# Optimization experiments

Measured on AMD Instinct MI355X. Metric: run time of the kernel, lower is better.

Reference implementation:

```python
import jax, jax.numpy as jnp
import numpy as np

B, T, V, E, H, L = 32, 128, 32000, 256, 256, 2


def setup_inputs() -> dict:
    key = jax.random.key(0)
    ks = jax.random.split(key, 9)
    s = 0.05  # weight scale to keep gates out of deep saturation
    x = jax.random.randint(ks[0], (B, T), 0, V, dtype=jnp.int32)
    return {
        "x": x,
        "embed_table": jax.random.normal(ks[1], (V, E), jnp.float32) * 0.1,
        "fW": jax.random.normal(ks[2], (L, E, 4 * H), jnp.float32) * s,
        "fU": jax.random.normal(ks[3], (L, H, 4 * H), jnp.float32) * s,
        "fb": jnp.zeros((L, 4 * H), jnp.float32),
        "bW": jax.random.normal(ks[4], (L, E, 4 * H), jnp.float32) * s,
        "bU": jax.random.normal(ks[5], (L, H, 4 * H), jnp.float32) * s,
        "bb": jnp.zeros((L, 4 * H), jnp.float32),
        "Wp": jax.random.normal(ks[6], (2 * H, V), jnp.float32) * s,
        "bp": jnp.zeros((V,), jnp.float32),
        "Wn": jax.random.normal(ks[7], ((T - 2) * 2 * H, 2), jnp.float32) * s,
        "bn": jnp.zeros((2,), jnp.float32),
    }


def run_stacked_lstm(emb, mask, W, U, b):
    """emb: [B,S,D], mask: [B,S] bool. Keras LSTMCell gate order (i,f,g,o);
    masked steps carry state through (output = previous top-layer h)."""
    nL = W.shape[0]
    Bz = emb.shape[0]
    Hd = U.shape[1]
    emb_t = jnp.swapaxes(emb, 0, 1)   # [S,B,D]
    mask_t = jnp.swapaxes(mask, 0, 1)  # [S,B]
    h0 = jnp.zeros((nL, Bz, Hd), emb.dtype)

    def step(carry, inp):
        hs, cs = carry
        x_t, m_t = inp
        m = m_t[:, None]
        new_h, new_c = [], []
        inp_x = x_t
        for l in range(nL):
            z = inp_x @ W[l] + hs[l] @ U[l] + b[l]
            i, f, g, o = jnp.split(z, 4, axis=-1)
            c = jax.nn.sigmoid(f) * cs[l] + jax.nn.sigmoid(i) * jnp.tanh(g)
            h = jax.nn.sigmoid(o) * jnp.tanh(c)
            h = jnp.where(m, h, hs[l])
            c = jnp.where(m, c, cs[l])
            new_h.append(h)
            new_c.append(c)
            inp_x = h
        return (jnp.stack(new_h), jnp.stack(new_c)), inp_x

    _, ys = jax.lax.scan(step, (h0, h0), (emb_t, mask_t))
    return jnp.swapaxes(ys, 0, 1)  # [B,S,H]


def reference(x, embed_table, fW, fU, fb, bW, bU, bb, Wp, bp, Wn, bn):
    o = embed_table[x]            # [B,T,E]
    mask = x != 0                 # mask_zero=True
    # forward LSTM over tokens 0..T-2
    f = run_stacked_lstm(o[:, :-1], mask[:, :-1], fW, fU, fb)
    # backward LSTM (go_backwards=True): run over reversed o[:,1:];
    # Keras RNN leaves outputs in reversed-time order.
    b_out = run_stacked_lstm(o[:, 1:][:, ::-1], mask[:, 1:][:, ::-1], bW, bU, bb)
    ctx = jnp.concatenate([f[:, :-1], b_out[:, 1:]], axis=-1)  # [B,T-2,2H]
    word_logits = ctx @ Wp + bp                                 # [B,T-2,V]
    nsp_logits = ctx.reshape(ctx.shape[0], -1) @ Wn + bn        # [B,2]
    return word_logits, nsp_logits
```

## Files before the change

kernel.cpp:

```cpp
#include <hip/hip_runtime.h>
#include <stdint.h>

typedef __bf16 bf16;
typedef __bf16 bf16x8 __attribute__((ext_vector_type(8)));
typedef float  f32x4  __attribute__((ext_vector_type(4)));

#define NB 16
#define OFF_CTR    0
#define CTR_BYTES  (4*128*4)
#define OFF_HIST   2048
#define HIST_ONE   (128*32*256*2)
#define OFF_H0F    (OFF_HIST)
#define OFF_H0B    (OFF_HIST + 1*HIST_ONE)
#define OFF_H1F    (OFF_HIST + 2*HIST_ONE)
#define OFF_H1B    (OFF_HIST + 3*HIST_ONE)
#define OFF_XF     (OFF_HIST + 4*HIST_ONE)
#define XF_BYTES   (4064*256*2)
#define OFF_XB     (OFF_XF + XF_BYTES)
#define OFF_FW0T   (OFF_XB + XF_BYTES)
#define W0T_BYTES  (1024*256*2)
#define OFF_BW0T   (OFF_FW0T + W0T_BYTES)
#define OFF_PRE0F  (OFF_BW0T + W0T_BYTES)
#define PRE_BYTES  (4064*1024*4)
#define OFF_PRE0B  (OFF_PRE0F + PRE_BYTES)
#define OFF_WPT    (OFF_PRE0B + PRE_BYTES)
#define WPT_BYTES  (32000*512*2)
#define OFF_CTX    (OFF_WPT + WPT_BYTES)
#define CTX_BYTES  (4032*512*2)
#define OFF_MF     (OFF_CTX + CTX_BYTES)
#define OFF_MB     (OFF_MF + 4096)

__device__ __forceinline__ int swz8(int row, int kblk) { return (kblk ^ (row & 7)) << 3; }

__device__ __forceinline__ uint64_t sys_load_u64(const uint64_t* p) {
  return __hip_atomic_load(p, __ATOMIC_RELAXED, __HIP_MEMORY_SCOPE_SYSTEM);
}
__device__ __forceinline__ void sys_store_u16(unsigned short* p, unsigned short v) {
  __hip_atomic_store(p, v, __ATOMIC_RELAXED, __HIP_MEMORY_SCOPE_SYSTEM);
}
__device__ __forceinline__ int sys_load_i32(const int* p) {
  return __hip_atomic_load(p, __ATOMIC_RELAXED, __HIP_MEMORY_SCOPE_SYSTEM);
}
__device__ __forceinline__ void sys_store_i32(int* p, int v) {
  __hip_atomic_store(p, v, __ATOMIC_RELAXED, __HIP_MEMORY_SCOPE_SYSTEM);
}

__device__ __forceinline__ void wait_flags(const int* f, int want, int tid) {
  if (tid < NB) {
    int spins = 0;
    while (sys_load_i32(&f[tid]) < want) {
      if (++spins > (1<<16)) __builtin_amdgcn_s_sleep(2);
      if (spins > (1<<20)) break;
    }
  }
  __atomic_signal_fence(__ATOMIC_SEQ_CST);
  __syncthreads();
}

typedef __attribute__((address_space(1))) unsigned int as1_u32;
typedef __attribute__((address_space(3))) unsigned int as3_u32;
__device__ __forceinline__ void gload16(const void* g, void* l) {
  __builtin_amdgcn_global_load_lds((as1_u32*)g, (as3_u32*)l, 16, 0, 0);
}

__global__ __launch_bounds__(256) void embed_kernel(
    const int* __restrict__ x, const float* __restrict__ tab,
    bf16* __restrict__ xf, bf16* __restrict__ xb,
    unsigned char* __restrict__ mf, unsigned char* __restrict__ mb)
{
  int t = blockIdx.x;
  int b = blockIdx.y;
  int k = threadIdx.x;
  int tokf = x[b*128 + t];
  int tokb = x[b*128 + 127 - t];
  xf[(size_t)(t*32+b)*256 + k] = (bf16)tab[(size_t)tokf*256 + k];
  xb[(size_t)(t*32+b)*256 + k] = (bf16)tab[(size_t)tokb*256 + k];
  if (k == 0) { mf[t*32+b] = (tokf != 0); mb[t*32+b] = (tokb != 0); }
}

__global__ __launch_bounds__(256) void transpose_to_bf16(
    const float* __restrict__ in, bf16* __restrict__ out, int R, int C)
{
  __shared__ float tile[64][65];
  int c0 = blockIdx.x*64, r0 = blockIdx.y*64;
  int tid = threadIdx.x;
  int r = tid >> 2, cs = (tid & 3)*16;
  #pragma unroll
  for (int i = 0; i < 16; i += 4) {
    float4 v = *(const float4*)(in + (size_t)(r0+r)*C + c0 + cs + i);
    tile[r][cs+i+0]=v.x; tile[r][cs+i+1]=v.y; tile[r][cs+i+2]=v.z; tile[r][cs+i+3]=v.w;
  }
  __syncthreads();
  int c = tid >> 2, rs = (tid & 3)*16;
  #pragma unroll
  for (int i = 0; i < 16; ++i)
    out[(size_t)(c0+c)*R + r0 + rs + i] = (bf16)tile[rs+i][c];
}

__global__ __launch_bounds__(256) void gemm_bf16(
    const bf16* __restrict__ A, const bf16* __restrict__ BT,
    const float* __restrict__ bias, float* __restrict__ C,
    int M, int N, int K)
{
  __shared__ bf16 As[128][64];
  __shared__ bf16 Bs[128][64];
  int tid = threadIdx.x;
  int row0 = blockIdx.x*128, col0 = blockIdx.y*128;
  int wave = tid >> 6, lane = tid & 63, l15 = lane & 15, quad = lane >> 4;
  int wm = (wave & 1)*64, wn = (wave >> 1)*64;
  int lr = lane >> 3;
  int lc = (lane & 7)*8;
  f32x4 acc[4][4] = {};
  for (int kk = 0; kk < K; kk += 64) {
    #pragma unroll
    for (int i = 0; i < 4; ++i) {
      int rb = (wave*4 + i)*8;
      int ga = row0 + rb + lr; if (ga > M-1) ga = M-1;
      gload16(A  + (size_t)ga*K + kk + lc,                 &As[rb][0]);
      gload16(BT + (size_t)(col0 + rb + lr)*K + kk + lc,   &Bs[rb][0]);
    }
    __syncthreads();
    #pragma unroll
    for (int ks = 0; ks < 64; ks += 32) {
      bf16x8 af[4], bfr[4];
      #pragma unroll
      for (int mi = 0; mi < 4; ++mi) af[mi]  = *(const bf16x8*)&As[wm + mi*16 + l15][ks + quad*8];
      #pragma unroll
      for (int ni = 0; ni < 4; ++ni) bfr[ni] = *(const bf16x8*)&Bs[wn + ni*16 + l15][ks + quad*8];
      #pragma unroll
      for (int mi = 0; mi < 4; ++mi)
        #pragma unroll
        for (int ni = 0; ni < 4; ++ni)
          acc[mi][ni] = __builtin_amdgcn_mfma_f32_16x16x32_bf16(af[mi], bfr[ni], acc[mi][ni], 0, 0, 0);
    }
    __syncthreads();
  }
  #pragma unroll
  for (int ni = 0; ni < 4; ++ni) {
    int col = col0 + wn + ni*16 + l15;
    float bv = bias[col];
    #pragma unroll
    for (int mi = 0; mi < 4; ++mi) {
      int rbase = row0 + wm + mi*16 + quad*4;
      #pragma unroll
      for (int r = 0; r < 4; ++r) {
        int grow = rbase + r;
        if (grow < M) C[(size_t)grow*N + col] = acc[mi][ni][r] + bv;
      }
    }
  }
}

__global__ __launch_bounds__(512) void recur_kernel(
    const float* __restrict__ pre0f, const float* __restrict__ pre0b,
    const float* __restrict__ fU0, const float* __restrict__ bU0,
    const float* __restrict__ fW1, const float* __restrict__ fU1,
    const float* __restrict__ bW1, const float* __restrict__ bU1,
    const float* __restrict__ fb1, const float* __restrict__ bb1,
    const unsigned char* __restrict__ mf, const unsigned char* __restrict__ mb,
    bf16* __restrict__ h0f, bf16* __restrict__ h0b,
    bf16* __restrict__ h1f, bf16* __restrict__ h1b,
    int* __restrict__ ctr)
{
  __shared__ bf16 U_T[64][512];
  __shared__ bf16 hA[32][512];
  __shared__ float z_s[32][65];

  int tid = threadIdx.x;
  int bx = blockIdx.x;
  int dir = bx >> 5, stage = (bx >> 4) & 1, blk = bx & 15;
  int j0 = blk * 16;
  const float* pre = dir ? pre0b : pre0f;
  const unsigned char* mgl = dir ? mb : mf;
  bf16* h0 = dir ? h0b : h0f;
  bf16* h1 = dir ? h1b : h1f;
  int* f0 = ctr + (dir*2 + 0)*16;
  int* f1 = ctr + (dir*2 + 1)*16;

  if (stage == 0) {
    const float* U = dir ? bU0 : fU0;
    for (int idx = tid; idx < 64*256; idx += 512) {
      int k = idx >> 6, c = idx & 63;
      int gc = (c >> 4)*256 + j0 + (c & 15);
      U_T[c][swz8(c, k >> 3) | (k & 7)] = (bf16)U[(size_t)k*1024 + gc];
    }
  } else {
    const float* W = dir ? bW1 : fW1;
    const float* U = dir ? bU1 : fU1;
    for (int idx = tid; idx < 64*512; idx += 512) {
      int k = idx >> 6, c = idx & 63;
      int gc = (c >> 4)*256 + j0 + (c & 15);
      float v = (k < 256) ? W[(size_t)k*1024 + gc] : U[(size_t)(k-256)*1024 + gc];
      U_T[c][swz8(c, k >> 3) | (k & 7)] = (bf16)v;
    }
  }
  int gb = tid & 31, gu = tid >> 5;
  float c_state = 0.f, h_state = 0.f;
  float bi = 0.f, bff = 0.f, bgg = 0.f, boo = 0.f;
  if (stage == 1) {
    const float* bias = dir ? bb1 : fb1;
    bi  = bias[0*256 + j0 + gu];
    bff = bias[1*256 + j0 + gu];
    bgg = bias[2*256 + j0 + gu];
    boo = bias[3*256 + j0 + gu];
  }
  int wave = tid >> 6, lane = tid & 63, l15 = lane & 15, quad = lane >> 4;
  int m0 = (wave & 1)*16, n0 = (wave >> 1)*16;
  __syncthreads();

  for (int t = 0; t < 127; ++t) {
    float p_i = bi, p_f = bff, p_g = bgg, p_o = boo;
    if (stage == 0) {
      const float* p = pre + ((size_t)t*32 + gb)*1024 + j0 + gu;
      p_i = p[0]; p_f = p[256]; p_g = p[512]; p_o = p[768];
    }
    unsigned char msk = mgl[t*32 + gb];
    f32x4 acc = {0.f, 0.f, 0.f, 0.f};

    if (stage == 0) {
      if (t > 0) wait_flags(f0, t, tid);
      const uint64_t* src = (const uint64_t*)(h0 + (size_t)t*8192);
      #pragma unroll
      for (int i = 0; i < 4; ++i) {
        int q = i*512 + tid;
        int r = q >> 6, seg = q & 63;
        uint64_t v = sys_load_u64(src + q);
        *(uint64_t*)&hA[r][swz8(r, seg >> 1) + (seg & 1)*4] = v;
      }
      __syncthreads();
      for (int kc = 0; kc < 256; kc += 32) {
        int kb = (kc >> 3) + quad;
        bf16x8 a = *(const bf16x8*)&hA[m0 + l15][swz8(m0 + l15, kb)];
        bf16x8 w = *(const bf16x8*)&U_T[n0 + l15][swz8(n0 + l15, kb)];
        acc = __builtin_amdgcn_mfma_f32_16x16x32_bf16(a, w, acc, 0, 0, 0);
      }
    } else {
      wait_flags(f0, t+1, tid);
      const uint64_t* s0p = (const uint64_t*)(h0 + (size_t)(t+1)*8192);
      #pragma unroll
      for (int i = 0; i < 4; ++i) {
        int q = i*512 + tid;
        int r = q >> 6, seg = q & 63;
        uint64_t v = sys_load_u64(s0p + q);
        *(uint64_t*)&hA[r][swz8(r, seg >> 1) + (seg & 1)*4] = v;
      }
      __syncthreads();
      for (int kc = 0; kc < 256; kc += 32) {
        int kb = (kc >> 3) + quad;
        bf16x8 a = *(const bf16x8*)&hA[m0 + l15][swz8(m0 + l15, kb)];
        bf16x8 w = *(const bf16x8*)&U_T[n0 + l15][swz8(n0 + l15, kb)];
        acc = __builtin_amdgcn_mfma_f32_16x16x32_bf16(a, w, acc, 0, 0, 0);
      }
      if (t > 0) wait_flags(f1, t, tid);
      const uint64_t* s1p = (const uint64_t*)(h1 + (size_t)t*8192);
      #pragma unroll
      for (int i = 0; i < 4; ++i) {
        int q = i*512 + tid;
        int r = q >> 6, seg = q & 63;
        uint64_t v = sys_load_u64(s1p + q);
        *(uint64_t*)&hA[r][swz8(r, (seg >> 1) + 32) + (seg & 1)*4] = v;
      }
      __syncthreads();
      for (int kc = 256; kc < 512; kc += 32) {
        int kb = (kc >> 3) + quad;
        bf16x8 a = *(const bf16x8*)&hA[m0 + l15][swz8(m0 + l15, kb)];
        bf16x8 w = *(const bf16x8*)&U_T[n0 + l15][swz8(n0 + l15, kb)];
        acc = __builtin_amdgcn_mfma_f32_16x16x32_bf16(a, w, acc, 0, 0, 0);
      }
    }

    #pragma unroll
    for (int r = 0; r < 4; ++r) z_s[m0 + quad*4 + r][n0 + l15] = acc[r];
    __syncthreads();

    float zi = z_s[gb][ 0 + gu] + p_i;
    float zf = z_s[gb][16 + gu] + p_f;
    float zg = z_s[gb][32 + gu] + p_g;
    float zo = z_s[gb][48 + gu] + p_o;
    float ig = 1.f/(1.f + expf(-zi));
    float fg = 1.f/(1.f + expf(-zf));
    float gg = tanhf(zg);
    float og = 1.f/(1.f + expf(-zo));
    float cn = fg*c_state + ig*gg;
    float hn = og*tanhf(cn);
    if (msk) { c_state = cn; h_state = hn; }

    bf16 hv = (bf16)h_state;
    unsigned short hb;
    __builtin_memcpy(&hb, &hv, 2);
    unsigned short* dst = (unsigned short*)((stage == 0 ? h0 : h1) + (size_t)(t+1)*8192 + gb*256 + j0 + gu);
    sys_store_u16(dst, hb);
    asm volatile("s_waitcnt vmcnt(0)" ::: "memory");
    __syncthreads();
    if (tid == 0) {
      __atomic_signal_fence(__ATOMIC_SEQ_CST);
      sys_store_i32(stage == 0 ? &f0[blk] : &f1[blk], t+1);
    }
  }
}

__global__ __launch_bounds__(256) void ctx_kernel(
    const bf16* __restrict__ h1f, const bf16* __restrict__ h1b, bf16* __restrict__ ctx)
{
  int tau = blockIdx.x;
  int b = blockIdx.y;
  int k = threadIdx.x;
  size_t r = (size_t)(b*126 + tau)*512;
  ctx[r + k]       = h1f[(size_t)(tau+1)*8192 + b*256 + k];
  ctx[r + 256 + k] = h1b[(size_t)(tau+2)*8192 + b*256 + k];
}

__global__ __launch_bounds__(256) void nsp_kernel(
    const bf16* __restrict__ ctx, const float* __restrict__ Wn,
    const float* __restrict__ bn, float* __restrict__ out)
{
  int b = blockIdx.x, tid = threadIdx.x;
  const unsigned short* cb = (const unsigned short*)ctx;
  float a0 = 0.f, a1 = 0.f;
  for (int flat = tid; flat < 64512; flat += 256) {
    int tau = flat >> 9, k = flat & 511;
    float cv = __uint_as_float((unsigned)cb[(size_t)(b*126 + tau)*512 + k] << 16);
    float2 w = *(const float2*)(Wn + 2*(size_t)flat);
    a0 += cv*w.x; a1 += cv*w.y;
  }
  __shared__ float r0[256], r1[256];
  r0[tid] = a0; r1[tid] = a1;
  __syncthreads();
  for (int s = 128; s > 0; s >>= 1) {
    if (tid < s) { r0[tid] += r0[tid+s]; r1[tid] += r1[tid+s]; }
    __syncthreads();
  }
  if (tid == 0) { out[b*2+0] = r0[0] + bn[0]; out[b*2+1] = r1[0] + bn[1]; }
}

extern "C" void kernel_launch(void* const* d_in, const int* in_sizes, int n_in,
                              void* d_out, int out_size, void* d_ws, size_t ws_size,
                              hipStream_t stream)
{
  const int*   x   = (const int*)d_in[0];
  const float* tab = (const float*)d_in[1];
  const float* fW  = (const float*)d_in[2];
  const float* fU  = (const float*)d_in[3];
  const float* fb  = (const float*)d_in[4];
  const float* bW  = (const float*)d_in[5];
  const float* bU  = (const float*)d_in[6];
  const float* bb  = (const float*)d_in[7];
  const float* Wp  = (const float*)d_in[8];
  const float* bp  = (const float*)d_in[9];
  const float* Wn  = (const float*)d_in[10];
  const float* bn  = (const float*)d_in[11];
  float* out = (float*)d_out;
  char* ws = (char*)d_ws;

  int*  ctr   = (int*)(ws + OFF_CTR);
  bf16* h0f   = (bf16*)(ws + OFF_H0F);
  bf16* h0b   = (bf16*)(ws + OFF_H0B);
  bf16* h1f   = (bf16*)(ws + OFF_H1F);
  bf16* h1b   = (bf16*)(ws + OFF_H1B);
  bf16* xf    = (bf16*)(ws + OFF_XF);
  bf16* xb    = (bf16*)(ws + OFF_XB);
  bf16* fW0T  = (bf16*)(ws + OFF_FW0T);
  bf16* bW0T  = (bf16*)(ws + OFF_BW0T);
  float* pre0f = (float*)(ws + OFF_PRE0F);
  float* pre0b = (float*)(ws + OFF_PRE0B);
  bf16* WpT   = (bf16*)(ws + OFF_WPT);
  bf16* ctx   = (bf16*)(ws + OFF_CTX);
  unsigned char* mf = (unsigned char*)(ws + OFF_MF);
  unsigned char* mb = (unsigned char*)(ws + OFF_MB);

  hipMemsetAsync(ws + OFF_CTR, 0, CTR_BYTES, stream);
  hipMemsetAsync(ws + OFF_H0F, 0, 16384, stream);
  hipMemsetAsync(ws + OFF_H0B, 0, 16384, stream);
  hipMemsetAsync(ws + OFF_H1F, 0, 16384, stream);
  hipMemsetAsync(ws + OFF_H1B, 0, 16384, stream);

  embed_kernel<<<dim3(127, 32), 256, 0, stream>>>(x, tab, xf, xb, mf, mb);

  transpose_to_bf16<<<dim3(16, 4),  256, 0, stream>>>(fW, fW0T, 256, 1024);
  transpose_to_bf16<<<dim3(16, 4),  256, 0, stream>>>(bW, bW0T, 256, 1024);
  transpose_to_bf16<<<dim3(500, 8), 256, 0, stream>>>(Wp, WpT, 512, 32000);

  gemm_bf16<<<dim3(32, 8), 256, 0, stream>>>(xf, fW0T, fb, pre0f, 4064, 1024, 256);
  gemm_bf16<<<dim3(32, 8), 256, 0, stream>>>(xb, bW0T, bb, pre0b, 4064, 1024, 256);

  recur_kernel<<<64, 512, 0, stream>>>(
      pre0f, pre0b,
      fU, bU,
      fW + 262144, fU + 262144, bW + 262144, bU + 262144,
      fb + 1024, bb + 1024,
      mf, mb, h0f, h0b, h1f, h1b, ctr);

  ctx_kernel<<<dim3(126, 32), 256, 0, stream>>>(h1f, h1b, ctx);

  gemm_bf16<<<dim3(32, 250), 256, 0, stream>>>(ctx, WpT, bp, out, 4032, 32000, 512);

  nsp_kernel<<<32, 256, 0, stream>>>(ctx, Wn, bn, out + (size_t)4032*32000);
}
```

Measured before the change: 1.677 ms.

## Replace per-step flag barriers with timestep-tagged hidden-state words in LSTM recurrence

The recurrent kernel no longer uses separate counter flags plus a store-drain and block barrier each step. Each hidden value is now written as a 32-bit word carrying the timestep tag, and consumers spin directly on the tagged data, which removes a round trip of flag publication per step. The MFMA accumulation is split into two independent chains, and the workspace is reorganised so the Wp transpose runs after the recurrence, reusing the pre-activation buffers. This doubles the hidden-history footprint, requires a larger memset, and relies on 64-bit loads observing both tagged halves consistently.

```diff
diff --git a/kernel.cpp b/kernel.cpp
--- a/kernel.cpp
+++ b/kernel.cpp
@@ -6,15 +6,14 @@
 typedef float  f32x4  __attribute__((ext_vector_type(4)));
 
 #define NB 16
-#define OFF_CTR    0
-#define CTR_BYTES  (4*128*4)
-#define OFF_HIST   2048
-#define HIST_ONE   (128*32*256*2)
-#define OFF_H0F    (OFF_HIST)
-#define OFF_H0B    (OFF_HIST + 1*HIST_ONE)
-#define OFF_H1F    (OFF_HIST + 2*HIST_ONE)
-#define OFF_H1B    (OFF_HIST + 3*HIST_ONE)
-#define OFF_XF     (OFF_HIST + 4*HIST_ONE)
+#define OFF_MF     0
+#define OFF_MB     4096
+#define OFF_H0F    8192
+#define TAG_ONE    (128*32*256*4)
+#define OFF_H0B    (OFF_H0F + 1*TAG_ONE)
+#define OFF_H1F    (OFF_H0F + 2*TAG_ONE)
+#define OFF_H1B    (OFF_H0F + 3*TAG_ONE)
+#define OFF_XF     (OFF_H0F + 4*TAG_ONE)
 #define XF_BYTES   (4064*256*2)
 #define OFF_XB     (OFF_XF + XF_BYTES)
 #define OFF_FW0T   (OFF_XB + XF_BYTES)
@@ -23,38 +22,16 @@
 #define OFF_PRE0F  (OFF_BW0T + W0T_BYTES)
 #define PRE_BYTES  (4064*1024*4)
 #define OFF_PRE0B  (OFF_PRE0F + PRE_BYTES)
-#define OFF_WPT    (OFF_PRE0B + PRE_BYTES)
-#define WPT_BYTES  (32000*512*2)
-#define OFF_CTX    (OFF_WPT + WPT_BYTES)
-#define CTX_BYTES  (4032*512*2)
-#define OFF_MF     (OFF_CTX + CTX_BYTES)
-#define OFF_MB     (OFF_MF + 4096)
+#define OFF_WPT    OFF_PRE0F
+#define OFF_CTX    OFF_XF
 
 __device__ __forceinline__ int swz8(int row, int kblk) { return (kblk ^ (row & 7)) << 3; }
 
 __device__ __forceinline__ uint64_t sys_load_u64(const uint64_t* p) {
   return __hip_atomic_load(p, __ATOMIC_RELAXED, __HIP_MEMORY_SCOPE_SYSTEM);
 }
-__device__ __forceinline__ void sys_store_u16(unsigned short* p, unsigned short v) {
+__device__ __forceinline__ void sys_store_u32(uint32_t* p, uint32_t v) {
   __hip_atomic_store(p, v, __ATOMIC_RELAXED, __HIP_MEMORY_SCOPE_SYSTEM);
-}
-__device__ __forceinline__ int sys_load_i32(const int* p) {
-  return __hip_atomic_load(p, __ATOMIC_RELAXED, __HIP_MEMORY_SCOPE_SYSTEM);
-}
-__device__ __forceinline__ void sys_store_i32(int* p, int v) {
-  __hip_atomic_store(p, v, __ATOMIC_RELAXED, __HIP_MEMORY_SCOPE_SYSTEM);
-}
-
-__device__ __forceinline__ void wait_flags(const int* f, int want, int tid) {
-  if (tid < NB) {
-    int spins = 0;
-    while (sys_load_i32(&f[tid]) < want) {
-      if (++spins > (1<<16)) __builtin_amdgcn_s_sleep(2);
-      if (spins > (1<<20)) break;
-    }
-  }
-  __atomic_signal_fence(__ATOMIC_SEQ_CST);
-  __syncthreads();
 }
 
 typedef __attribute__((address_space(1))) unsigned int as1_u32;
@@ -158,9 +135,8 @@
     const float* __restrict__ bW1, const float* __restrict__ bU1,
     const float* __restrict__ fb1, const float* __restrict__ bb1,
     const unsigned char* __restrict__ mf, const unsigned char* __restrict__ mb,
-    bf16* __restrict__ h0f, bf16* __restrict__ h0b,
-    bf16* __restrict__ h1f, bf16* __restrict__ h1b,
-    int* __restrict__ ctr)
+    uint32_t* __restrict__ h0f, uint32_t* __restrict__ h0b,
+    uint32_t* __restrict__ h1f, uint32_t* __restrict__ h1b)
 {
   __shared__ bf16 U_T[64][512];
   __shared__ bf16 hA[32][512];
@@ -172,10 +148,9 @@
   int j0 = blk * 16;
   const float* pre = dir ? pre0b : pre0f;
   const unsigned char* mgl = dir ? mb : mf;
-  bf16* h0 = dir ? h0b : h0f;
-  bf16* h1 = dir ? h1b : h1f;
-  int* f0 = ctr + (dir*2 + 0)*16;
-  int* f1 = ctr + (dir*2 + 1)*16;
+  uint32_t* h0 = dir ? h0b : h0f;
+  uint32_t* h1 = dir ? h1b : h1f;
+  uint32_t* hout = stage ? h1 : h0;
 
   if (stage == 0) {
     const float* U = dir ? bU0 : fU0;
@@ -194,7 +169,8 @@
       U_T[c][swz8(c, k >> 3) | (k & 7)] = (bf16)v;
     }
   }
-  int gb = tid & 31, gu = tid >> 5;
+
+  int gb = tid >> 4, gu = tid & 15;
   float c_state = 0.f, h_state = 0.f;
   float bi = 0.f, bff = 0.f, bgg = 0.f, boo = 0.f;
   if (stage == 1) {
@@ -206,6 +182,17 @@
   }
   int wave = tid >> 6, lane = tid & 63, l15 = lane & 15, quad = lane >> 4;
   int m0 = (wave & 1)*16, n0 = (wave >> 1)*16;
+
+  int laddr[16];
+  #pragma unroll
+  for (int j = 0; j < 16; ++j) {
+    int g = (j & 7)*512 + tid;
+    int kb = g >> 8, rem = g & 255;
+    int row = rem >> 3, up = (rem & 7)*2;
+    int p = (j >> 3)*256 + kb*16 + up;
+    laddr[j] = row*512 + swz8(row, p >> 3) + (p & 7);
+  }
+  bf16* hAf = &hA[0][0];
   __syncthreads();
 
   for (int t = 0; t < 127; ++t) {
@@ -215,62 +202,112 @@
       p_i = p[0]; p_f = p[256]; p_g = p[512]; p_o = p[768];
     }
     unsigned char msk = mgl[t*32 + gb];
-    f32x4 acc = {0.f, 0.f, 0.f, 0.f};
-
+
+    uint64_t v[16];
     if (stage == 0) {
-      if (t > 0) wait_flags(f0, t, tid);
-      const uint64_t* src = (const uint64_t*)(h0 + (size_t)t*8192);
-      #pragma unroll
-      for (int i = 0; i < 4; ++i) {
-        int q = i*512 + tid;
-        int r = q >> 6, seg = q & 63;
-        uint64_t v = sys_load_u64(src + q);
-        *(uint64_t*)&hA[r][swz8(r, seg >> 1) + (seg & 1)*4] = v;
-      }
-      __syncthreads();
-      for (int kc = 0; kc < 256; kc += 32) {
-        int kb = (kc >> 3) + quad;
-        bf16x8 a = *(const bf16x8*)&hA[m0 + l15][swz8(m0 + l15, kb)];
-        bf16x8 w = *(const bf16x8*)&U_T[n0 + l15][swz8(n0 + l15, kb)];
-        acc = __builtin_amdgcn_mfma_f32_16x16x32_bf16(a, w, acc, 0, 0, 0);
+      const uint64_t* s0 = (const uint64_t*)h0 + (size_t)t*4096;
+      if (t > 0) {
+        #pragma unroll
+        for (int j = 0; j < 8; ++j) v[j] = sys_load_u64(s0 + (j*512 + tid));
+        uint64_t pat = ((uint64_t)t << 48) | ((uint64_t)t << 16);
+        #pragma unroll
+        for (int j = 0; j < 8; ++j) {
+          int sp = 0;
+          while ((v[j] & 0xFFFF0000FFFF0000ull) != pat) {
+            if (++sp > 1024) __builtin_amdgcn_s_sleep(2);
+            if (sp > (1<<22)) break;
+            v[j] = sys_load_u64(s0 + (j*512 + tid));
+          }
+        }
+      } else {
+        #pragma unroll
+        for (int j = 0; j < 8; ++j) v[j] = 0;
+      }
+      #pragma unroll
+      for (int j = 0; j < 8; ++j) {
+        uint32_t pk = (uint32_t)(v[j] & 0xFFFF) | ((uint32_t)((v[j] >> 32) & 0xFFFF) << 16);
+        *(uint32_t*)&hAf[laddr[j]] = pk;
       }
     } else {
-      wait_flags(f0, t+1, tid);
-      const uint64_t* s0p = (const uint64_t*)(h0 + (size_t)(t+1)*8192);
-      #pragma unroll
-      for (int i = 0; i < 4; ++i) {
-        int q = i*512 + tid;
-        int r = q >> 6, seg = q & 63;
-        uint64_t v = sys_load_u64(s0p + q);
-        *(uint64_t*)&hA[r][swz8(r, seg >> 1) + (seg & 1)*4] = v;
-      }
-      __syncthreads();
-      for (int kc = 0; kc < 256; kc += 32) {
-        int kb = (kc >> 3) + quad;
-        bf16x8 a = *(const bf16x8*)&hA[m0 + l15][swz8(m0 + l15, kb)];
-        bf16x8 w = *(const bf16x8*)&U_T[n0 + l15][swz8(n0 + l15, kb)];
-        acc = __builtin_amdgcn_mfma_f32_16x16x32_bf16(a, w, acc, 0, 0, 0);
-      }
-      if (t > 0) wait_flags(f1, t, tid);
-      const uint64_t* s1p = (const uint64_t*)(h1 + (size_t)t*8192);
-      #pragma unroll
-      for (int i = 0; i < 4; ++i) {
-        int q = i*512 + tid;
-        int r = q >> 6, seg = q & 63;
-        uint64_t v = sys_load_u64(s1p + q);
-        *(uint64_t*)&hA[r][swz8(r, (seg >> 1) + 32) + (seg & 1)*4] = v;
-      }
-      __syncthreads();
-      for (int kc = 256; kc < 512; kc += 32) {
-        int kb = (kc >> 3) + quad;
-        bf16x8 a = *(const bf16x8*)&hA[m0 + l15][swz8(m0 + l15, kb)];
-        bf16x8 w = *(const bf16x8*)&U_T[n0 + l15][swz8(n0 + l15, kb)];
-        acc = __builtin_amdgcn_mfma_f32_16x16x32_bf16(a, w, acc, 0, 0, 0);
-      }
-    }
-
+      const uint64_t* s0 = (const uint64_t*)h0 + (size_t)(t+1)*4096;
+      const uint64_t* s1 = (const uint64_t*)h1 + (size_t)t*4096;
+      #pragma unroll
+      for (int j = 0; j < 8; ++j) v[j] = sys_load_u64(s0 + (j*512 + tid));
+      if (t > 0) {
+        #pragma unroll
+        for (int j = 8; j < 16; ++j) v[j] = sys_load_u64(s1 + ((j-8)*512 + tid));
+      } else {
+        #pragma unroll
+        for (int j = 8; j < 16; ++j) v[j] = 0;
+      }
+      uint64_t pat0 = ((uint64_t)(t+1) << 48) | ((uint64_t)(t+1) << 16);
+      #pragma unroll
+      for (int j = 0; j < 8; ++j) {
+        int sp = 0;
+        while ((v[j] & 0xFFFF0000FFFF0000ull) != pat0) {
+          if (++sp > 1024) __builtin_amdgcn_s_sleep(2);
+          if (sp > (1<<22)) break;
+          v[j] = sys_load_u64(s0 + (j*512 + tid));
+        }
+      }
+      if (t > 0) {
+        uint64_t pat1 = ((uint64_t)t << 48) | ((uint64_t)t << 16);
+        #pragma unroll
+        for (int j = 8; j < 16; ++j) {
+          int sp = 0;
+          while ((v[j] & 0xFFFF0000FFFF0000ull) != pat1) {
+            if (++sp > 1024) __builtin_amdgcn_s_sleep(2);
+            if (sp > (1<<22)) break;
+            v[j] = sys_load_u64(s1 + ((j-8)*512 + tid));
+          }
+        }
+      }
+      #pragma unroll
+      for (int j = 0; j < 16; ++j) {
+        uint32_t pk = (uint32_t)(v[j] & 0xFFFF) | ((uint32_t)((v[j] >> 32) & 0xFFFF) << 16);
+        *(uint32_t*)&hAf[laddr[j]] = pk;
+      }
+    }
+    __syncthreads();
+
+    f32x4 zac;
+    {
+      f32x4 a0 = {0.f,0.f,0.f,0.f}, a1 = {0.f,0.f,0.f,0.f};
+      if (stage == 0) {
+        #pragma unroll
+        for (int kc = 0; kc < 128; kc += 32) {
+          int kb = (kc >> 3) + quad;
+          a0 = __builtin_amdgcn_mfma_f32_16x16x32_bf16(
+                 *(const bf16x8*)&hA[m0 + l15][swz8(m0 + l15, kb)],
+                 *(const bf16x8*)&U_T[n0 + l15][swz8(n0 + l15, kb)], a0, 0, 0, 0);
+        }
+        #pragma unroll
+        for (int kc = 128; kc < 256; kc += 32) {
+          int kb = (kc >> 3) + quad;
+          a1 = __builtin_amdgcn_mfma_f32_16x16x32_bf16(
+                 *(const bf16x8*)&hA[m0 + l15][swz8(m0 + l15, kb)],
+                 *(const bf16x8*)&U_T[n0 + l15][swz8(n0 + l15, kb)], a1, 0, 0, 0);
+        }
+      } else {
+        #pragma unroll
+        for (int kc = 0; kc < 256; kc += 32) {
+          int kb = (kc >> 3) + quad;
+          a0 = __builtin_amdgcn_mfma_f32_16x16x32_bf16(
+                 *(const bf16x8*)&hA[m0 + l15][swz8(m0 + l15, kb)],
+                 *(const bf16x8*)&U_T[n0 + l15][swz8(n0 + l15, kb)], a0, 0, 0, 0);
+        }
+        #pragma unroll
+        for (int kc = 256; kc < 512; kc += 32) {
+          int kb = (kc >> 3) + quad;
+          a1 = __builtin_amdgcn_mfma_f32_16x16x32_bf16(
+                 *(const bf16x8*)&hA[m0 + l15][swz8(m0 + l15, kb)],
+                 *(const bf16x8*)&U_T[n0 + l15][swz8(n0 + l15, kb)], a1, 0, 0, 0);
+        }
+      }
+      zac = a0 + a1;
+    }
     #pragma unroll
-    for (int r = 0; r < 4; ++r) z_s[m0 + quad*4 + r][n0 + l15] = acc[r];
+    for (int r = 0; r < 4; ++r) z_s[m0 + quad*4 + r][n0 + l15] = zac[r];
     __syncthreads();
 
     float zi = z_s[gb][ 0 + gu] + p_i;
@@ -288,26 +325,22 @@
     bf16 hv = (bf16)h_state;
     unsigned short hb;
     __builtin_memcpy(&hb, &hv, 2);
-    unsigned short* dst = (unsigned short*)((stage == 0 ? h0 : h1) + (size_t)(t+1)*8192 + gb*256 + j0 + gu);
-    sys_store_u16(dst, hb);
-    asm volatile("s_waitcnt vmcnt(0)" ::: "memory");
-    __syncthreads();
-    if (tid == 0) {
-      __atomic_signal_fence(__ATOMIC_SEQ_CST);
-      sys_store_i32(stage == 0 ? &f0[blk] : &f1[blk], t+1);
-    }
+    uint32_t val = ((uint32_t)(t+1) << 16) | (uint32_t)hb;
+    sys_store_u32(hout + (size_t)(t+1)*8192 + blk*512 + tid, val);
   }
 }
 
 __global__ __launch_bounds__(256) void ctx_kernel(
-    const bf16* __restrict__ h1f, const bf16* __restrict__ h1b, bf16* __restrict__ ctx)
+    const uint32_t* __restrict__ h1f, const uint32_t* __restrict__ h1b, bf16* __restrict__ ctx)
 {
   int tau = blockIdx.x;
   int b = blockIdx.y;
   int k = threadIdx.x;
   size_t r = (size_t)(b*126 + tau)*512;
-  ctx[r + k]       = h1f[(size_t)(tau+1)*8192 + b*256 + k];
-  ctx[r + 256 + k] = h1b[(size_t)(tau+2)*8192 + b*256 + k];
+  uint32_t vf = h1f[(size_t)(tau+1)*8192 + (k>>4)*512 + b*16 + (k&15)];
+  uint32_t vb = h1b[(size_t)(tau+2)*8192 + (k>>4)*512 + b*16 + (k&15)];
+  ((unsigned short*)ctx)[r + k]       = (unsigned short)(vf & 0xFFFF);
+  ((unsigned short*)ctx)[r + 256 + k] = (unsigned short)(vb & 0xFFFF);
 }
 
 __global__ __launch_bounds__(256) void nsp_kernel(
@@ -352,11 +385,12 @@
   float* out = (float*)d_out;
   char* ws = (char*)d_ws;
 
-  int*  ctr   = (int*)(ws + OFF_CTR);
-  bf16* h0f   = (bf16*)(ws + OFF_H0F);
-  bf16* h0b   = (bf16*)(ws + OFF_H0B);
-  bf16* h1f   = (bf16*)(ws + OFF_H1F);
-  bf16* h1b   = (bf16*)(ws + OFF_H1B);
+  unsigned char* mf = (unsigned char*)(ws + OFF_MF);
+  unsigned char* mb = (unsigned char*)(ws + OFF_MB);
+  uint32_t* h0f = (uint32_t*)(ws + OFF_H0F);
+  uint32_t* h0b = (uint32_t*)(ws + OFF_H0B);
+  uint32_t* h1f = (uint32_t*)(ws + OFF_H1F);
+  uint32_t* h1b = (uint32_t*)(ws + OFF_H1B);
   bf16* xf    = (bf16*)(ws + OFF_XF);
   bf16* xb    = (bf16*)(ws + OFF_XB);
   bf16* fW0T  = (bf16*)(ws + OFF_FW0T);
@@ -365,20 +399,13 @@
   float* pre0b = (float*)(ws + OFF_PRE0B);
   bf16* WpT   = (bf16*)(ws + OFF_WPT);
   bf16* ctx   = (bf16*)(ws + OFF_CTX);
-  unsigned char* mf = (unsigned char*)(ws + OFF_MF);
-  unsigned char* mb = (unsigned char*)(ws + OFF_MB);
-
-  hipMemsetAsync(ws + OFF_CTR, 0, CTR_BYTES, stream);
-  hipMemsetAsync(ws + OFF_H0F, 0, 16384, stream);
-  hipMemsetAsync(ws + OFF_H0B, 0, 16384, stream);
-  hipMemsetAsync(ws + OFF_H1F, 0, 16384, stream);
-  hipMemsetAsync(ws + OFF_H1B, 0, 16384, stream);
+
+  hipMemsetAsync(ws + OFF_H0F, 0, 4*(size_t)TAG_ONE, stream);
 
   embed_kernel<<<dim3(127, 32), 256, 0, stream>>>(x, tab, xf, xb, mf, mb);
 
   transpose_to_bf16<<<dim3(16, 4),  256, 0, stream>>>(fW, fW0T, 256, 1024);
   transpose_to_bf16<<<dim3(16, 4),  256, 0, stream>>>(bW, bW0T, 256, 1024);
-  transpose_to_bf16<<<dim3(500, 8), 256, 0, stream>>>(Wp, WpT, 512, 32000);
 
   gemm_bf16<<<dim3(32, 8), 256, 0, stream>>>(xf, fW0T, fb, pre0f, 4064, 1024, 256);
   gemm_bf16<<<dim3(32, 8), 256, 0, stream>>>(xb, bW0T, bb, pre0b, 4064, 1024, 256);
@@ -388,7 +415,9 @@
       fU, bU,
       fW + 262144, fU + 262144, bW + 262144, bU + 262144,
       fb + 1024, bb + 1024,
-      mf, mb, h0f, h0b, h1f, h1b, ctr);
+      mf, mb, h0f, h0b, h1f, h1b);
+
+  transpose_to_bf16<<<dim3(500, 8), 256, 0, stream>>>(Wp, WpT, 512, 32000);
 
   ctx_kernel<<<dim3(126, 32), 256, 0, stream>>>(h1f, h1b, ctx);
 
```

Result: faster. 1.487 ms (-11.4%).
